# Performance work log

Measured on AMD Instinct MI355X. Metric: run time of the kernel, lower is better.

The kernel has to match this reference:

```python
import jax, jax.numpy as jnp
import numpy as np
import math

B, L = 32, 1000
N_CHAR, EMB, D_MODEL, N_HEADS, PRED_HS, N_OUT = 256, 512, 512, 8, 512, 8
D_HEAD = D_MODEL // N_HEADS


def _pos_encoding(seq_len, d_model, dtype=jnp.float32):
    pos = jnp.arange(seq_len, dtype=dtype)[:, None]                      # [L,1]
    div = jnp.exp(jnp.arange(0, d_model, 2, dtype=dtype) * (-math.log(10000.0) / d_model))
    pe = jnp.zeros((seq_len, d_model), dtype=dtype)
    pe = pe.at[:, 0::2].set(jnp.sin(pos * div))
    pe = pe.at[:, 1::2].set(jnp.cos(pos * div))
    return pe                                                            # [L,D]


def setup_inputs() -> dict:
    key = jax.random.key(0)
    ks = jax.random.split(key, 12)
    def xavier(k, shape):
        fan_in, fan_out = shape[1], shape[0]
        lim = math.sqrt(6.0 / (fan_in + fan_out))
        return jax.random.uniform(k, shape, jnp.float32, -lim, lim)
    data = jax.random.randint(ks[0], (B, L), 0, N_CHAR, dtype=jnp.int64)
    lengths = jnp.clip(jax.random.randint(ks[1], (B,), 0, L, dtype=jnp.int64), 1, L)
    emb = jax.random.normal(ks[2], (N_CHAR, EMB), jnp.float32) * math.sqrt(2.0 / (N_CHAR + EMB))
    return {
        'data': data,
        'lengths': lengths,
        'emb': emb,
        'Wq': xavier(ks[3], (D_MODEL, EMB)), 'bq': jnp.zeros((D_MODEL,), jnp.float32),
        'Wk': xavier(ks[4], (D_MODEL, EMB)), 'bk': jnp.zeros((D_MODEL,), jnp.float32),
        'Wv': xavier(ks[5], (D_MODEL, EMB)), 'bv': jnp.zeros((D_MODEL,), jnp.float32),
        'W1': xavier(ks[6], (PRED_HS, D_MODEL)), 'b1': jnp.full((PRED_HS,), 0.01, jnp.float32),
        'W2': xavier(ks[7], (N_OUT, PRED_HS)), 'b2': jnp.full((N_OUT,), 0.01, jnp.float32),
    }


def reference(data, lengths, emb, Wq, bq, Wk, bk, Wv, bv, W1, b1, W2, b2):
    bs, seq = data.shape
    x = emb[data]                                              # [B,L,E]
    x = x + _pos_encoding(seq, x.shape[-1], x.dtype)[None]     # positional encoding
    # q/k/v projections -> [B,L,H,dh]
    q = (x @ Wq.T + bq).reshape(bs, seq, N_HEADS, D_HEAD)
    k = (x @ Wk.T + bk).reshape(bs, seq, N_HEADS, D_HEAD)
    v = (x @ Wv.T + bv).reshape(bs, seq, N_HEADS, D_HEAD)
    scale = 1.0 / math.sqrt(D_HEAD)
    score = jnp.einsum('bqhd,bkhd->bhqk', q, k) * scale        # [B,H,L,L]
    causal = jnp.tril(jnp.ones((seq, seq), dtype=bool))        # True = keep
    score = jnp.where(causal[None, None], score, -jnp.inf)
    attn = jax.nn.softmax(score, axis=-1)
    ctx = jnp.einsum('bhqk,bkhd->bqhd', attn, v).reshape(bs, seq, D_MODEL)
    # take hidden state at last valid position per sequence
    ctx_last = jnp.take_along_axis(ctx, (lengths - 1)[:, None, None].astype(jnp.int32), axis=1)[:, 0]  # [B,D]
    h = jax.nn.leaky_relu(ctx_last @ W1.T + b1)                # pred layer 1
    out = jax.nn.relu(h @ W2.T + b2)                           # [B,8]
    out = jnp.mean(out, axis=-1)                               # [B]
    return jax.nn.leaky_relu(out)
```

## Files before the change

kernel.cpp:

```cpp
#include <hip/hip_runtime.h>
#include <math.h>

#define BATCH   32
#define LSEQ    1000
#define NHEADS  8
#define DHEAD   64
#define PE_C    (-9.210340371976184f / 512.0f)

__device__ __forceinline__ float pe_val(int j, int e) {
  int ef = e & ~1;
  float dv  = __expf((float)ef * PE_C);
  float arg = (float)j * dv;
  return (e & 1) ? __cosf(arg) : __sinf(arg);
}

__global__ __launch_bounds__(256) void qfold_kernel(
    const int* __restrict__ data, const int* __restrict__ lengths,
    const float* __restrict__ emb,
    const float* __restrict__ Wq, const float* __restrict__ bq,
    const float* __restrict__ Wk, const float* __restrict__ bk,
    float* __restrict__ wfT4, float* __restrict__ bias_dot) {
  int h = blockIdx.x, b = blockIdx.y;
  int p = lengths[b] - 1;
  int t = threadIdx.x;
  __shared__ float xs[512];
  __shared__ float red[256];
  __shared__ float qs[64];
  int tok = data[b * LSEQ + p];
  const float* er = emb + (size_t)tok * 512;
  xs[t]       = er[t]       + pe_val(p, t);
  xs[t + 256] = er[t + 256] + pe_val(p, t + 256);
  __syncthreads();
  int col = h * 64 + (t & 63);
  int kp  = t >> 6;
  {
    const float* wr = Wq + (size_t)col * 512 + kp * 128;
    const float* xp = xs + kp * 128;
    float a = 0.0f;
    for (int e = 0; e < 128; e += 4) {
      float4 wv = *(const float4*)(wr + e);
      a += wv.x * xp[e] + wv.y * xp[e + 1] + wv.z * xp[e + 2] + wv.w * xp[e + 3];
    }
    red[t] = a;
  }
  __syncthreads();
  if (t < 64) {
    float qval = (red[t] + red[t + 64] + red[t + 128] + red[t + 192]
                  + bq[h * 64 + t]) * 0.125f;
    qs[t] = qval;
    float bd = qval * bk[h * 64 + t];
    #pragma unroll
    for (int o = 32; o > 0; o >>= 1) bd += __shfl_xor(bd, o, 64);
    if (t == 0) bias_dot[b * NHEADS + h] = bd;
  }
  __syncthreads();
  float a0 = 0.0f, a1 = 0.0f;
  const float* wkb = Wk + (size_t)(h * 64) * 512;
  for (int d = 0; d < 64; ++d) {
    float qd = qs[d];
    a0 += qd * wkb[d * 512 + t];
    a1 += qd * wkb[d * 512 + t + 256];
  }
  int bh = b * NHEADS + h;
  int e1 = t, e2 = t + 256;
  wfT4[(e1 >> 2) * 1024 + bh * 4 + (e1 & 3)] = a0;
  wfT4[(e2 >> 2) * 1024 + bh * 4 + (e2 & 3)] = a1;
}

__global__ __launch_bounds__(256) void foldmd_kernel(
    const float* __restrict__ emb, const float* __restrict__ wfT4,
    float* __restrict__ MD) {
  __shared__ float rows[2][512];
  int t  = threadIdx.x;
  int rr = t >> 7;
  int e0 = (t & 127) * 4;
  int rg = blockIdx.x * 2 + rr;
  if (rg < 256) {
    float4 v = *(const float4*)(emb + (size_t)rg * 512 + e0);
    *(float4*)(&rows[rr][e0]) = v;
  } else {
    int j = rg - 256;
    float4 v;
    float dv0 = __expf((float)e0 * PE_C);
    float dv1 = __expf((float)(e0 + 2) * PE_C);
    float a0 = (float)j * dv0, a1 = (float)j * dv1;
    v.x = __sinf(a0); v.y = __cosf(a0);
    v.z = __sinf(a1); v.w = __cosf(a1);
    *(float4*)(&rows[rr][e0]) = v;
  }
  __syncthreads();
  float acc0 = 0.0f, acc1 = 0.0f;
  #pragma unroll 8
  for (int g = 0; g < 128; ++g) {
    float4 w4 = *(const float4*)(wfT4 + g * 1024 + t * 4);
    float4 r0 = *(const float4*)(&rows[0][4 * g]);
    float4 r1 = *(const float4*)(&rows[1][4 * g]);
    acc0 += r0.x * w4.x + r0.y * w4.y + r0.z * w4.z + r0.w * w4.w;
    acc1 += r1.x * w4.x + r1.y * w4.y + r1.z * w4.z + r1.w * w4.w;
  }
  MD[(size_t)(blockIdx.x * 2)     * 256 + t] = acc0;
  MD[(size_t)(blockIdx.x * 2 + 1) * 256 + t] = acc1;
}

__global__ __launch_bounds__(256) void attn_kernel(
    const int* __restrict__ data, const int* __restrict__ lengths,
    const float* __restrict__ MD, const float* __restrict__ bias_dot,
    float* __restrict__ probs, float* __restrict__ sums) {
  int h = blockIdx.x, b = blockIdx.y;
  int bh = b * NHEADS + h;
  int n = lengths[b];
  int t = threadIdx.x;
  __shared__ float redm[4];
  __shared__ float redsum[4];
  const float* Edot = MD;
  const float* Pdot = MD + 256 * 256;
  float bd = bias_dot[bh];
  float sreg[4];
  int   nit = 0;
  float lmax = -INFINITY;
  for (int j = t; j < n; j += 256) {
    int tok = data[b * LSEQ + j];
    float s = Edot[tok * 256 + bh] + Pdot[(size_t)j * 256 + bh] + bd;
    sreg[nit++] = s;
    lmax = fmaxf(lmax, s);
  }
  #pragma unroll
  for (int o = 32; o > 0; o >>= 1) lmax = fmaxf(lmax, __shfl_xor(lmax, o, 64));
  if ((t & 63) == 0) redm[t >> 6] = lmax;
  __syncthreads();
  float gmax = fmaxf(fmaxf(redm[0], redm[1]), fmaxf(redm[2], redm[3]));
  float ls = 0.0f;
  {
    int it = 0;
    for (int j = t; j < n; j += 256) {
      float e = __expf(sreg[it++] - gmax);
      probs[(size_t)bh * 1024 + j] = e;
      ls += e;
    }
  }
  #pragma unroll
  for (int o = 32; o > 0; o >>= 1) ls += __shfl_xor(ls, o, 64);
  if ((t & 63) == 0) redsum[t >> 6] = ls;
  __syncthreads();
  if (t == 0) sums[bh] = redsum[0] + redsum[1] + redsum[2] + redsum[3];
}

__global__ __launch_bounds__(256) void ypass_kernel(
    const int* __restrict__ data, const int* __restrict__ lengths,
    const float* __restrict__ emb, const float* __restrict__ probs,
    float* __restrict__ y_part) {
  int jc = blockIdx.x, b = blockIdx.y;
  int n = lengths[b];
  int j0 = jc * 125;
  if (j0 >= n) return;
  int cnt = min(125, n - j0);
  int t = threadIdx.x;
  __shared__ float pl[128][8];
  __shared__ int   tk[128];
  if (t < cnt) {
    tk[t] = data[b * LSEQ + j0 + t];
    #pragma unroll
    for (int h = 0; h < 8; ++h)
      pl[t][h] = probs[(size_t)(b * NHEADS + h) * 1024 + j0 + t];
  }
  __syncthreads();
  int w = t >> 6, lane = t & 63;
  int e0 = w * 128 + lane * 2;
  float dv = __expf((float)e0 * PE_C);
  float acc0[8] = {0,0,0,0,0,0,0,0};
  float acc1[8] = {0,0,0,0,0,0,0,0};
  for (int jj = 0; jj < cnt; ++jj) {
    int tok = tk[jj];
    float2 ev = *(const float2*)(emb + (size_t)tok * 512 + e0);
    float arg = (float)(j0 + jj) * dv;
    float x0 = ev.x + __sinf(arg);
    float x1 = ev.y + __cosf(arg);
    #pragma unroll
    for (int h = 0; h < 8; ++h) {
      float pj = pl[jj][h];
      acc0[h] += pj * x0;
      acc1[h] += pj * x1;
    }
  }
  size_t base = (size_t)(b * 8 + jc) * 4096 + e0;
  #pragma unroll
  for (int h = 0; h < 8; ++h) {
    float2 o; o.x = acc0[h]; o.y = acc1[h];
    *(float2*)(y_part + base + h * 512) = o;
  }
}

__global__ __launch_bounds__(256) void ctx_kernel(
    const int* __restrict__ lengths, const float* __restrict__ y_part,
    const float* __restrict__ sums, const float* __restrict__ Wv,
    const float* __restrict__ bv, float* __restrict__ ctx) {
  int h = blockIdx.x, b = blockIdx.y;
  int t = threadIdx.x;
  __shared__ float ys[512];
  __shared__ float red[256];
  int n = lengths[b];
  int nc = (n + 124) / 125;
  float inv = 1.0f / sums[b * NHEADS + h];
  float s0 = 0.0f, s1 = 0.0f;
  for (int jc = 0; jc < nc; ++jc) {
    size_t base = (size_t)(b * 8 + jc) * 4096 + h * 512;
    s0 += y_part[base + t];
    s1 += y_part[base + t + 256];
  }
  ys[t]       = s0 * inv;
  ys[t + 256] = s1 * inv;
  __syncthreads();
  int col = h * 64 + (t & 63);
  int kp  = t >> 6;
  const float* wr = Wv + (size_t)col * 512 + kp * 128;
  const float* xp = ys + kp * 128;
  float a = 0.0f;
  for (int e = 0; e < 128; e += 4) {
    float4 wv4 = *(const float4*)(wr + e);
    a += wv4.x * xp[e] + wv4.y * xp[e + 1] + wv4.z * xp[e + 2] + wv4.w * xp[e + 3];
  }
  red[t] = a;
  __syncthreads();
  if (t < 64)
    ctx[b * 512 + h * 64 + t] =
        red[t] + red[t + 64] + red[t + 128] + red[t + 192] + bv[h * 64 + t];
}

__global__ __launch_bounds__(256) void mlp1_kernel(
    const float* __restrict__ ctx, const float* __restrict__ W1,
    const float* __restrict__ b1, float* __restrict__ hs) {
  int chunk = blockIdx.x, b = blockIdx.y;
  int t = threadIdx.x;
  __shared__ float xs[512];
  __shared__ float red[256];
  xs[t]       = ctx[b * 512 + t];
  xs[t + 256] = ctx[b * 512 + t + 256];
  __syncthreads();
  int col = chunk * 64 + (t & 63);
  int kp  = t >> 6;
  const float* wr = W1 + (size_t)col * 512 + kp * 128;
  const float* xp = xs + kp * 128;
  float a = 0.0f;
  for (int e = 0; e < 128; e += 4) {
    float4 wv = *(const float4*)(wr + e);
    a += wv.x * xp[e] + wv.y * xp[e + 1] + wv.z * xp[e + 2] + wv.w * xp[e + 3];
  }
  red[t] = a;
  __syncthreads();
  if (t < 64) {
    float v = red[t] + red[t + 64] + red[t + 128] + red[t + 192] + b1[chunk * 64 + t];
    hs[b * 512 + chunk * 64 + t] = (v > 0.0f) ? v : 0.01f * v;
  }
}

__global__ __launch_bounds__(256) void mlp2_kernel(
    const float* __restrict__ hs, const float* __restrict__ W2,
    const float* __restrict__ b2, float* __restrict__ out) {
  int b = blockIdx.x, t = threadIdx.x;
  __shared__ float o8[8];
  int j = t >> 5, sub = t & 31;
  const float* hr  = hs + (size_t)b * 512;
  const float* w2r = W2 + (size_t)j * 512;
  float part = 0.0f;
  for (int e = sub * 16; e < sub * 16 + 16; e += 4) {
    float4 wv = *(const float4*)(w2r + e);
    float4 hv = *(const float4*)(hr + e);
    part += wv.x * hv.x + wv.y * hv.y + wv.z * hv.z + wv.w * hv.w;
  }
  #pragma unroll
  for (int o = 16; o > 0; o >>= 1) part += __shfl_xor(part, o, 64);
  if (sub == 0) o8[j] = fmaxf(part + b2[j], 0.0f);
  __syncthreads();
  if (t == 0) {
    float m = 0.0f;
    #pragma unroll
    for (int i = 0; i < 8; ++i) m += o8[i];
    m *= 0.125f;
    out[b] = (m > 0.0f) ? m : 0.01f * m;
  }
}

extern "C" void kernel_launch(void* const* d_in, const int* in_sizes, int n_in,
                              void* d_out, int out_size, void* d_ws, size_t ws_size,
                              hipStream_t stream) {
  const int*   data    = (const int*)d_in[0];
  const int*   lengths = (const int*)d_in[1];
  const float* emb     = (const float*)d_in[2];
  const float* Wq      = (const float*)d_in[3];
  const float* bq      = (const float*)d_in[4];
  const float* Wk      = (const float*)d_in[5];
  const float* bk      = (const float*)d_in[6];
  const float* Wv      = (const float*)d_in[7];
  const float* bv      = (const float*)d_in[8];
  const float* W1      = (const float*)d_in[9];
  const float* b1      = (const float*)d_in[10];
  const float* W2      = (const float*)d_in[11];
  const float* b2      = (const float*)d_in[12];
  float* out = (float*)d_out;

  char* ws = (char*)d_ws;
  float* wfT4     = (float*)(ws);
  float* MD       = (float*)(ws + 524288);
  float* bias_dot = (float*)(ws + 1810432);
  float* probs    = (float*)(ws + 1811456);
  float* sums     = (float*)(ws + 2860032);
  float* y_part   = (float*)(ws + 2861056);
  float* ctx      = (float*)(ws + 7055360);
  float* hs       = (float*)(ws + 7120896);

  dim3 g1(NHEADS, BATCH);
  qfold_kernel<<<g1, 256, 0, stream>>>(data, lengths, emb, Wq, bq, Wk, bk,
                                       wfT4, bias_dot);
  foldmd_kernel<<<628, 256, 0, stream>>>(emb, wfT4, MD);
  dim3 g3(NHEADS, BATCH);
  attn_kernel<<<g3, 256, 0, stream>>>(data, lengths, MD, bias_dot, probs, sums);
  dim3 g4(8, BATCH);
  ypass_kernel<<<g4, 256, 0, stream>>>(data, lengths, emb, probs, y_part);
  dim3 g5(NHEADS, BATCH);
  ctx_kernel<<<g5, 256, 0, stream>>>(lengths, y_part, sums, Wv, bv, ctx);
  dim3 g6(8, BATCH);
  mlp1_kernel<<<g6, 256, 0, stream>>>(ctx, W1, b1, hs);
  mlp2_kernel<<<BATCH, 256, 0, stream>>>(hs, W2, b2, out);
}
```

Measured before the change: 148.6 us.

## Fuse softmax into y-pass with chunked online-softmax merge in ctx kernel

Merges the attention-score/softmax kernel into the y-pass kernel. Each chunk block now computes its own local max and sum over its 125 positions, stores them in an mS buffer, and keeps the unnormalized probabilities in shared memory. The ctx kernel rescales and combines the per-chunk partials, flash-attention style, which removes one launch and the probs round trip through global memory. foldmd is retiled to 8 rows by 64 bh per block and folds the bias into the embedding rows, at the cost of recomputing sin/exp per block tile.

```diff
diff --git a/kernel.cpp b/kernel.cpp
--- a/kernel.cpp
+++ b/kernel.cpp
@@ -69,130 +69,148 @@
 
 __global__ __launch_bounds__(256) void foldmd_kernel(
     const float* __restrict__ emb, const float* __restrict__ wfT4,
-    float* __restrict__ MD) {
-  __shared__ float rows[2][512];
-  int t  = threadIdx.x;
-  int rr = t >> 7;
-  int e0 = (t & 127) * 4;
-  int rg = blockIdx.x * 2 + rr;
-  if (rg < 256) {
-    float4 v = *(const float4*)(emb + (size_t)rg * 512 + e0);
-    *(float4*)(&rows[rr][e0]) = v;
-  } else {
-    int j = rg - 256;
+    const float* __restrict__ bias_dot, float* __restrict__ MD) {
+  __shared__ float rows[8 * 512];
+  int t   = threadIdx.x;
+  int r0  = blockIdx.x * 8;
+  int bh0 = blockIdx.y * 64;
+  #pragma unroll
+  for (int i = 0; i < 4; ++i) {
+    int fi = t + i * 256;
+    int rr = fi >> 7;
+    int e  = (fi & 127) * 4;
+    int rg = r0 + rr;
     float4 v;
-    float dv0 = __expf((float)e0 * PE_C);
-    float dv1 = __expf((float)(e0 + 2) * PE_C);
-    float a0 = (float)j * dv0, a1 = (float)j * dv1;
-    v.x = __sinf(a0); v.y = __cosf(a0);
-    v.z = __sinf(a1); v.w = __cosf(a1);
-    *(float4*)(&rows[rr][e0]) = v;
-  }
-  __syncthreads();
-  float acc0 = 0.0f, acc1 = 0.0f;
+    if (rg < 256) {
+      v = *(const float4*)(emb + (size_t)rg * 512 + e);
+    } else {
+      int j = rg - 256;
+      float dv0 = __expf((float)e * PE_C);
+      float dv1 = __expf((float)(e + 2) * PE_C);
+      float a0 = (float)j * dv0, a1 = (float)j * dv1;
+      v.x = __sinf(a0); v.y = __cosf(a0);
+      v.z = __sinf(a1); v.w = __cosf(a1);
+    }
+    *(float4*)(&rows[rr * 512 + e]) = v;
+  }
+  __syncthreads();
+  int bh_l = t & 63;
+  int rp   = t >> 6;
+  const float* rw0 = rows + (2 * rp) * 512;
+  const float* rw1 = rows + (2 * rp + 1) * 512;
+  const float* wp  = wfT4 + (bh0 + bh_l) * 4;
+  float a0 = 0.0f, a1 = 0.0f;
   #pragma unroll 8
   for (int g = 0; g < 128; ++g) {
-    float4 w4 = *(const float4*)(wfT4 + g * 1024 + t * 4);
-    float4 r0 = *(const float4*)(&rows[0][4 * g]);
-    float4 r1 = *(const float4*)(&rows[1][4 * g]);
-    acc0 += r0.x * w4.x + r0.y * w4.y + r0.z * w4.z + r0.w * w4.w;
-    acc1 += r1.x * w4.x + r1.y * w4.y + r1.z * w4.z + r1.w * w4.w;
-  }
-  MD[(size_t)(blockIdx.x * 2)     * 256 + t] = acc0;
-  MD[(size_t)(blockIdx.x * 2 + 1) * 256 + t] = acc1;
-}
-
-__global__ __launch_bounds__(256) void attn_kernel(
+    float4 w4 = *(const float4*)(wp + g * 1024);
+    float4 v0 = *(const float4*)(rw0 + 4 * g);
+    float4 v1 = *(const float4*)(rw1 + 4 * g);
+    a0 += v0.x * w4.x + v0.y * w4.y + v0.z * w4.z + v0.w * w4.w;
+    a1 += v1.x * w4.x + v1.y * w4.y + v1.z * w4.z + v1.w * w4.w;
+  }
+  float bd = (r0 < 256) ? bias_dot[bh0 + bh_l] : 0.0f;
+  MD[(size_t)(r0 + 2 * rp)     * 256 + bh0 + bh_l] = a0 + bd;
+  MD[(size_t)(r0 + 2 * rp + 1) * 256 + bh0 + bh_l] = a1 + bd;
+}
+
+__global__ __launch_bounds__(256) void attn_ypass_kernel(
     const int* __restrict__ data, const int* __restrict__ lengths,
-    const float* __restrict__ MD, const float* __restrict__ bias_dot,
-    float* __restrict__ probs, float* __restrict__ sums) {
-  int h = blockIdx.x, b = blockIdx.y;
-  int bh = b * NHEADS + h;
-  int n = lengths[b];
-  int t = threadIdx.x;
-  __shared__ float redm[4];
-  __shared__ float redsum[4];
-  const float* Edot = MD;
-  const float* Pdot = MD + 256 * 256;
-  float bd = bias_dot[bh];
-  float sreg[4];
-  int   nit = 0;
-  float lmax = -INFINITY;
-  for (int j = t; j < n; j += 256) {
-    int tok = data[b * LSEQ + j];
-    float s = Edot[tok * 256 + bh] + Pdot[(size_t)j * 256 + bh] + bd;
-    sreg[nit++] = s;
-    lmax = fmaxf(lmax, s);
-  }
-  #pragma unroll
-  for (int o = 32; o > 0; o >>= 1) lmax = fmaxf(lmax, __shfl_xor(lmax, o, 64));
-  if ((t & 63) == 0) redm[t >> 6] = lmax;
-  __syncthreads();
-  float gmax = fmaxf(fmaxf(redm[0], redm[1]), fmaxf(redm[2], redm[3]));
-  float ls = 0.0f;
-  {
-    int it = 0;
-    for (int j = t; j < n; j += 256) {
-      float e = __expf(sreg[it++] - gmax);
-      probs[(size_t)bh * 1024 + j] = e;
-      ls += e;
-    }
-  }
-  #pragma unroll
-  for (int o = 32; o > 0; o >>= 1) ls += __shfl_xor(ls, o, 64);
-  if ((t & 63) == 0) redsum[t >> 6] = ls;
-  __syncthreads();
-  if (t == 0) sums[bh] = redsum[0] + redsum[1] + redsum[2] + redsum[3];
-}
-
-__global__ __launch_bounds__(256) void ypass_kernel(
-    const int* __restrict__ data, const int* __restrict__ lengths,
-    const float* __restrict__ emb, const float* __restrict__ probs,
-    float* __restrict__ y_part) {
+    const float* __restrict__ emb, const float* __restrict__ MD,
+    float* __restrict__ mS, float* __restrict__ y_part) {
   int jc = blockIdx.x, b = blockIdx.y;
   int n = lengths[b];
   int j0 = jc * 125;
   if (j0 >= n) return;
   int cnt = min(125, n - j0);
   int t = threadIdx.x;
-  __shared__ float pl[128][8];
-  __shared__ int   tk[128];
-  if (t < cnt) {
-    tk[t] = data[b * LSEQ + j0 + t];
-    #pragma unroll
-    for (int h = 0; h < 8; ++h)
-      pl[t][h] = probs[(size_t)(b * NHEADS + h) * 1024 + j0 + t];
-  }
-  __syncthreads();
-  int w = t >> 6, lane = t & 63;
-  int e0 = w * 128 + lane * 2;
-  float dv = __expf((float)e0 * PE_C);
+  __shared__ float sl[125][8];
+  __shared__ int   tk[125];
+  __shared__ float redw[4][8];
+  __shared__ float m_sh[8], s_sh[8];
+  const float* Edot = MD;
+  const float* Pdot = MD + 256 * 256;
+  if (t < 125) {
+    if (t < cnt) {
+      int tok = data[b * LSEQ + j0 + t];
+      tk[t] = tok;
+      const float* er = Edot + (size_t)tok * 256 + b * 8;
+      const float* pr = Pdot + (size_t)(j0 + t) * 256 + b * 8;
+      float4 e0 = *(const float4*)(er);
+      float4 e1 = *(const float4*)(er + 4);
+      float4 p0 = *(const float4*)(pr);
+      float4 p1 = *(const float4*)(pr + 4);
+      sl[t][0] = e0.x + p0.x; sl[t][1] = e0.y + p0.y;
+      sl[t][2] = e0.z + p0.z; sl[t][3] = e0.w + p0.w;
+      sl[t][4] = e1.x + p1.x; sl[t][5] = e1.y + p1.y;
+      sl[t][6] = e1.z + p1.z; sl[t][7] = e1.w + p1.w;
+    } else {
+      #pragma unroll
+      for (int h = 0; h < 8; ++h) sl[t][h] = -INFINITY;
+    }
+  }
+  __syncthreads();
+  int h = t & 7, jg = t >> 3, w = t >> 6;
+  {
+    float m = -INFINITY;
+    for (int j = jg; j < 125; j += 32) m = fmaxf(m, sl[j][h]);
+    #pragma unroll
+    for (int o = 8; o < 64; o <<= 1) m = fmaxf(m, __shfl_xor(m, o, 64));
+    if ((t & 63) < 8) redw[w][t & 7] = m;
+  }
+  __syncthreads();
+  if (t < 8)
+    m_sh[t] = fmaxf(fmaxf(redw[0][t], redw[1][t]),
+                    fmaxf(redw[2][t], redw[3][t]));
+  __syncthreads();
+  {
+    float mh = m_sh[h];
+    float sum = 0.0f;
+    for (int j = jg; j < 125; j += 32) {
+      float p = __expf(sl[j][h] - mh);
+      sl[j][h] = p;
+      sum += p;
+    }
+    #pragma unroll
+    for (int o = 8; o < 64; o <<= 1) sum += __shfl_xor(sum, o, 64);
+    if ((t & 63) < 8) redw[w][t & 7] = sum;
+  }
+  __syncthreads();
+  if (t < 8)
+    s_sh[t] = redw[0][t] + redw[1][t] + redw[2][t] + redw[3][t];
+  __syncthreads();
+  int lane = t & 63;
+  int e0i = w * 128 + lane * 2;
+  float dv = __expf((float)e0i * PE_C);
   float acc0[8] = {0,0,0,0,0,0,0,0};
   float acc1[8] = {0,0,0,0,0,0,0,0};
   for (int jj = 0; jj < cnt; ++jj) {
     int tok = tk[jj];
-    float2 ev = *(const float2*)(emb + (size_t)tok * 512 + e0);
+    float2 ev = *(const float2*)(emb + (size_t)tok * 512 + e0i);
     float arg = (float)(j0 + jj) * dv;
     float x0 = ev.x + __sinf(arg);
     float x1 = ev.y + __cosf(arg);
     #pragma unroll
-    for (int h = 0; h < 8; ++h) {
-      float pj = pl[jj][h];
-      acc0[h] += pj * x0;
-      acc1[h] += pj * x1;
-    }
-  }
-  size_t base = (size_t)(b * 8 + jc) * 4096 + e0;
+    for (int hh = 0; hh < 8; ++hh) {
+      float pj = sl[jj][hh];
+      acc0[hh] += pj * x0;
+      acc1[hh] += pj * x1;
+    }
+  }
+  size_t base = (size_t)(b * 8 + jc) * 4096 + e0i;
   #pragma unroll
-  for (int h = 0; h < 8; ++h) {
-    float2 o; o.x = acc0[h]; o.y = acc1[h];
-    *(float2*)(y_part + base + h * 512) = o;
+  for (int hh = 0; hh < 8; ++hh) {
+    float2 o; o.x = acc0[hh]; o.y = acc1[hh];
+    *(float2*)(y_part + base + hh * 512) = o;
+  }
+  if (t < 8) {
+    float2 ms; ms.x = m_sh[t]; ms.y = s_sh[t];
+    *(float2*)(mS + ((size_t)(b * 8 + jc) * 8 + t) * 2) = ms;
   }
 }
 
 __global__ __launch_bounds__(256) void ctx_kernel(
     const int* __restrict__ lengths, const float* __restrict__ y_part,
-    const float* __restrict__ sums, const float* __restrict__ Wv,
+    const float* __restrict__ mS, const float* __restrict__ Wv,
     const float* __restrict__ bv, float* __restrict__ ctx) {
   int h = blockIdx.x, b = blockIdx.y;
   int t = threadIdx.x;
@@ -200,13 +218,19 @@
   __shared__ float red[256];
   int n = lengths[b];
   int nc = (n + 124) / 125;
-  float inv = 1.0f / sums[b * NHEADS + h];
-  float s0 = 0.0f, s1 = 0.0f;
+  float M = -INFINITY;
+  for (int jc = 0; jc < nc; ++jc)
+    M = fmaxf(M, mS[((size_t)(b * 8 + jc) * 8 + h) * 2]);
+  float S = 0.0f, s0 = 0.0f, s1 = 0.0f;
   for (int jc = 0; jc < nc; ++jc) {
+    float2 ms = *(const float2*)(mS + ((size_t)(b * 8 + jc) * 8 + h) * 2);
+    float wgt = __expf(ms.x - M);
+    S += wgt * ms.y;
     size_t base = (size_t)(b * 8 + jc) * 4096 + h * 512;
-    s0 += y_part[base + t];
-    s1 += y_part[base + t + 256];
-  }
+    s0 += wgt * y_part[base + t];
+    s1 += wgt * y_part[base + t + 256];
+  }
+  float inv = 1.0f / S;
   ys[t]       = s0 * inv;
   ys[t + 256] = s1 * inv;
   __syncthreads();
@@ -302,23 +326,21 @@
   float* wfT4     = (float*)(ws);
   float* MD       = (float*)(ws + 524288);
   float* bias_dot = (float*)(ws + 1810432);
-  float* probs    = (float*)(ws + 1811456);
-  float* sums     = (float*)(ws + 2860032);
-  float* y_part   = (float*)(ws + 2861056);
-  float* ctx      = (float*)(ws + 7055360);
-  float* hs       = (float*)(ws + 7120896);
+  float* mS       = (float*)(ws + 1811456);
+  float* y_part   = (float*)(ws + 1827840);
+  float* ctx      = (float*)(ws + 6022144);
+  float* hs       = (float*)(ws + 6087680);
 
   dim3 g1(NHEADS, BATCH);
   qfold_kernel<<<g1, 256, 0, stream>>>(data, lengths, emb, Wq, bq, Wk, bk,
                                        wfT4, bias_dot);
-  foldmd_kernel<<<628, 256, 0, stream>>>(emb, wfT4, MD);
-  dim3 g3(NHEADS, BATCH);
-  attn_kernel<<<g3, 256, 0, stream>>>(data, lengths, MD, bias_dot, probs, sums);
-  dim3 g4(8, BATCH);
-  ypass_kernel<<<g4, 256, 0, stream>>>(data, lengths, emb, probs, y_part);
-  dim3 g5(NHEADS, BATCH);
-  ctx_kernel<<<g5, 256, 0, stream>>>(lengths, y_part, sums, Wv, bv, ctx);
-  dim3 g6(8, BATCH);
-  mlp1_kernel<<<g6, 256, 0, stream>>>(ctx, W1, b1, hs);
+  dim3 g2(157, 4);
+  foldmd_kernel<<<g2, 256, 0, stream>>>(emb, wfT4, bias_dot, MD);
+  dim3 g3(8, BATCH);
+  attn_ypass_kernel<<<g3, 256, 0, stream>>>(data, lengths, emb, MD, mS, y_part);
+  dim3 g4(NHEADS, BATCH);
+  ctx_kernel<<<g4, 256, 0, stream>>>(lengths, y_part, mS, Wv, bv, ctx);
+  dim3 g5(8, BATCH);
+  mlp1_kernel<<<g5, 256, 0, stream>>>(ctx, W1, b1, hs);
   mlp2_kernel<<<BATCH, 256, 0, stream>>>(hs, W2, b2, out);
 }
```

Measured after the change: 140.9 us, median of 2. 5.2% less time.
